# Kernel tuning notes

Measured on AMD Instinct MI355X. Metric: run time of the kernel, lower is better.

The kernel has to match this reference:

```python
import jax, jax.numpy as jnp
import numpy as np

H = 8
DA, DP, DK = 2048, 1024, 1024
B, N = 4, 2048
DOUT = 512
INNER = (DA + DP + DK) // H  # 512 = heads*dim_head


def setup_inputs() -> dict:
    key = jax.random.key(0)
    ks = jax.random.split(key, 7)
    x = jax.random.normal(ks[0], (B, N, DA + DP + DK), jnp.float32)
    mask = jax.random.randint(ks[1], (B, 1, N, N), 0, 2, jnp.int32)
    W_a = jax.random.normal(ks[2], (3 * DA // H, DA), jnp.float32) * (DA ** -0.5)
    W_p = jax.random.normal(ks[3], (3 * DP // H, DP), jnp.float32) * (DP ** -0.5)
    W_k = jax.random.normal(ks[4], (3 * DK // H, DK), jnp.float32) * (DK ** -0.5)
    W_out = jax.random.normal(ks[5], (DOUT, INNER), jnp.float32) * (INNER ** -0.5)
    b_out = jnp.zeros((DOUT,), jnp.float32)
    return {"x": x, "W_a": W_a, "W_p": W_p, "W_k": W_k,
            "W_out": W_out, "b_out": b_out, "mask": mask}


def _heads(t):  # [b, n, h*d] -> [b, h, n, d]
    b, n, hd = t.shape
    return t.reshape(b, n, H, hd // H).transpose(0, 2, 1, 3)


def reference(x, W_a, W_p, W_k, W_out, b_out, mask):
    # three branch QKV projections (each branch sees its own slice of x)
    qkv_a = x[..., :DA] @ W_a.T                      # [b, n, 3*DA/H]
    qkv_p = x[..., DA:DA + DP] @ W_p.T               # [b, n, 3*DP/H]
    qkv_k = x[..., DA + DP:] @ W_k.T                 # [b, n, 3*DK/H]
    q_a, k_a, v_a = [_heads(t) for t in jnp.split(qkv_a, 3, axis=-1)]
    q_p, k_p, v_p = [_heads(t) for t in jnp.split(qkv_p, 3, axis=-1)]
    q_k, k_k, v_k = [_heads(t) for t in jnp.split(qkv_k, 3, axis=-1)]

    m = mask > 0                                     # [b, 1, n, n]
    neg = jnp.asarray(-1e10, x.dtype)

    def branch(q, k, d):
        dots = jnp.einsum('bhid,bhjd->bhij', q, k) * (d ** -0.5)
        return jax.nn.softmax(jnp.where(m, dots, neg), axis=-1)

    # betas = [1,1,1] normalized -> 1/3 each (the nn.Parameters are unused in fwd)
    attn = (branch(q_a, k_a, DA) + branch(q_p, k_p, DP) + branch(q_k, k_k, DK)) / 3.0

    v = jnp.concatenate([v_a, v_p, v_k], axis=-1)    # [b, h, n, INNER/H]
    out = jnp.einsum('bhij,bhjd->bhid', attn, v)     # [b, h, n, INNER/H]
    out = out.transpose(0, 2, 1, 3).reshape(x.shape[0], x.shape[1], INNER)
    return out @ W_out.T + b_out
```

## Files before the change

kernel.cpp:

```cpp
#include <hip/hip_runtime.h>
#include <hip/hip_bf16.h>

typedef __attribute__((ext_vector_type(8))) __bf16 bf16x8;
typedef __attribute__((ext_vector_type(4))) float f32x4;
typedef unsigned short u16;
typedef unsigned int u32;
typedef unsigned long long u64;

__device__ __forceinline__ u32 cvtpk(float lo, float hi) {
  u32 r;
  asm("v_cvt_pk_bf16_f32 %0, %1, %2" : "=v"(r) : "v"(lo), "v"(hi));
  return r;
}
__device__ __forceinline__ float rexp2(float x) {
  float r;
  asm("v_exp_f32 %0, %1" : "=v"(r) : "v"(x));
  return r;
}
__device__ __forceinline__ void gl_lds16(const void* g, void* l) {
  __builtin_amdgcn_global_load_lds((const __attribute__((address_space(1))) void*)g,
                                   (__attribute__((address_space(3))) void*)l, 16, 0, 0);
}
__device__ __forceinline__ int sigma_inv(int n) {
  return ((n >> 5) << 5) | (((n & 15) >> 2) << 3) | ((n & 3) << 1) | ((n >> 4) & 1);
}

__global__ __launch_bounds__(256) void prep_kernel(
    const float* __restrict__ x, u16* __restrict__ xb,
    const float* __restrict__ Wa, const float* __restrict__ Wp,
    const float* __restrict__ Wk, const float* __restrict__ Wo,
    u16* __restrict__ Wab, u16* __restrict__ Wpb,
    u16* __restrict__ Wkb, u16* __restrict__ Wob,
    const int* __restrict__ mask, u64* __restrict__ bits, int xblocks) {
  int bid = blockIdx.x;
  if (bid < xblocks) {
    const int idx = (bid * 256 + threadIdx.x) * 16;
    const float4 a0 = *(const float4*)(x + idx);
    const float4 a1 = *(const float4*)(x + idx + 4);
    const float4 a2 = *(const float4*)(x + idx + 8);
    const float4 a3 = *(const float4*)(x + idx + 12);
    uint4 t0, t1;
    t0.x = cvtpk(a0.x, a0.y); t0.y = cvtpk(a0.z, a0.w);
    t0.z = cvtpk(a1.x, a1.y); t0.w = cvtpk(a1.z, a1.w);
    t1.x = cvtpk(a2.x, a2.y); t1.y = cvtpk(a2.z, a2.w);
    t1.z = cvtpk(a3.x, a3.y); t1.w = cvtpk(a3.z, a3.w);
    *(uint4*)(xb + idx) = t0;
    *(uint4*)(xb + idx + 8) = t1;
    return;
  }
  bid -= xblocks;
  if (bid < 2560) {
    const float* s; u16* d; int base;
    if (bid < 1536)      { s = Wa; d = Wab; base = bid; }
    else if (bid < 1920) { s = Wp; d = Wpb; base = bid - 1536; }
    else if (bid < 2304) { s = Wk; d = Wkb; base = bid - 1920; }
    else                 { s = Wo; d = Wob; base = bid - 2304; }
    const int idx = (base * 256 + threadIdx.x) * 4;
    const float4 v = *(const float4*)(s + idx);
    *(uint2*)(d + idx) = make_uint2(cvtpk(v.x, v.y), cvtpk(v.z, v.w));
    return;
  }
  bid -= 2560;
  const int lane = threadIdx.x & 63;
  const long long gw = (long long)bid * 4 + (threadIdx.x >> 6);
  const long long nwaves = 1024LL * 4;
  const long long nwords = 16777216LL / 64;
  for (long long i = gw; i < nwords; i += nwaves) {
    const int m = mask[i * 64 + lane];
    const u64 bal = __ballot(m > 0);
    if (lane == 0) bits[i] = bal;
  }
}

__device__ __forceinline__ void qk_store(
    float v0, float v1, float v2, float v3, int m_base, int c,
    int dhs, int seg, float fs,
    u16* __restrict__ Qb, u16* __restrict__ Kb) {
  const int which = c >> (3 + dhs);
  const float f = (which == 0) ? fs : 1.0f;
  const u32 r01 = cvtpk(v0 * f, v1 * f);
  const u32 r23 = cvtpk(v2 * f, v3 * f);
  const u16 bvv[4] = {(u16)r01, (u16)(r01 >> 16), (u16)r23, (u16)(r23 >> 16)};
  const int hd_mask = (8 << dhs) - 1;
  const int r = c & hd_mask;
  const int hh = r >> dhs;
  const int d = r & ((1 << dhs) - 1);
  #pragma unroll
  for (int j = 0; j < 4; ++j) {
    const int m = m_base + j;
    const int bb = m >> 11, n = m & 2047;
    const size_t bhn = (size_t)(bb * 8 + hh) * 2048 + n;
    const u16 bv = bvv[j];
    if (which == 0) Qb[bhn * 64 + seg + d] = bv;
    else            Kb[bhn * 64 + seg + d] = bv;
  }
}

__global__ __launch_bounds__(256) void qkv_gemm_kernel(
    const u16* __restrict__ xb, const u16* __restrict__ Wa,
    const u16* __restrict__ Wp, const u16* __restrict__ Wk,
    u16* __restrict__ Qb, u16* __restrict__ Kb, u16* __restrict__ Vt) {
  __shared__ u16 smem[64 * 64 + 128 * 64];
  u16* lA = smem;
  u16* lB = smem + 64 * 64;

  const int tid = threadIdx.x;
  const int w = tid >> 6, l = tid & 63;
  const int lr = l & 15, lg = l >> 4;

  const int wg = blockIdx.x;
  const int xcd = wg & 7;
  const int q = wg >> 3;
  const int mtl = q / 12, nt = q % 12;
  const int mt = (xcd << 4) + mtl;

  const u16* W; int xoff, Kd, col0, dhs, seg;
  if (nt < 6)      { W = Wa; xoff = 0;    Kd = 2048; col0 = nt * 128;       dhs = 5; seg = 0;  }
  else if (nt < 9) { W = Wp; xoff = 2048; Kd = 1024; col0 = (nt - 6) * 128; dhs = 4; seg = 32; }
  else             { W = Wk; xoff = 3072; Kd = 1024; col0 = (nt - 9) * 128; dhs = 4; seg = 48; }
  const float qscale = (dhs == 5) ? 0.031880107f : 0.045084220f;
  const bool isV = (nt == 4) | (nt == 5) | (nt == 8) | (nt == 11);

  const int m0 = mt * 64;
  f32x4 acc[4][2] = {};
  const int ubase = tid & ~63;

  const int nk = Kd >> 6;
  #pragma unroll 1
  for (int kt = 0; kt < nk; ++kt) {
    const int k0 = kt << 6;
    #pragma unroll
    for (int i = 0; i < 2; ++i) {
      const int ch = i * 256 + tid;
      const int row = ch >> 3, c8 = (ch & 7) << 3;
      gl_lds16(xb + (size_t)(m0 + row) * 4096 + xoff + k0 + c8,
               lA + (size_t)(i * 256 + ubase) * 8);
    }
    #pragma unroll
    for (int i = 0; i < 4; ++i) {
      const int ch = i * 256 + tid;
      const int row = ch >> 3, c8 = (ch & 7) << 3;
      gl_lds16(W + (size_t)(col0 + row) * Kd + k0 + c8,
               lB + (size_t)(i * 256 + ubase) * 8);
    }
    __syncthreads();
    bf16x8 af[4][2], bfr[2][2];
    #pragma unroll
    for (int mi = 0; mi < 4; ++mi) {
      af[mi][0] = *(const bf16x8*)(lA + (mi * 16 + lr) * 64 + lg * 8);
      af[mi][1] = *(const bf16x8*)(lA + (mi * 16 + lr) * 64 + 32 + lg * 8);
    }
    #pragma unroll
    for (int ni = 0; ni < 2; ++ni) {
      bfr[ni][0] = *(const bf16x8*)(lB + (w * 32 + ni * 16 + lr) * 64 + lg * 8);
      bfr[ni][1] = *(const bf16x8*)(lB + (w * 32 + ni * 16 + lr) * 64 + 32 + lg * 8);
    }
    #pragma unroll
    for (int mi = 0; mi < 4; ++mi)
      #pragma unroll
      for (int ni = 0; ni < 2; ++ni) {
        acc[mi][ni] = __builtin_amdgcn_mfma_f32_16x16x32_bf16(af[mi][0], bfr[ni][0], acc[mi][ni], 0, 0, 0);
        acc[mi][ni] = __builtin_amdgcn_mfma_f32_16x16x32_bf16(af[mi][1], bfr[ni][1], acc[mi][ni], 0, 0, 0);
      }
    __syncthreads();
  }

  if (!isV) {
    #pragma unroll
    for (int mi = 0; mi < 4; ++mi)
      #pragma unroll
      for (int ni = 0; ni < 2; ++ni)
        qk_store(acc[mi][ni][0], acc[mi][ni][1], acc[mi][ni][2], acc[mi][ni][3],
                 m0 + mi * 16 + lg * 4, col0 + w * 32 + ni * 16 + lr,
                 dhs, seg, qscale, Qb, Kb);
  } else {
    #pragma unroll
    for (int mi = 0; mi < 4; ++mi)
      #pragma unroll
      for (int ni = 0; ni < 2; ++ni) {
        const u32 r01 = cvtpk(acc[mi][ni][0], acc[mi][ni][1]);
        const u32 r23 = cvtpk(acc[mi][ni][2], acc[mi][ni][3]);
        const u16 bvv[4] = {(u16)r01, (u16)(r01 >> 16), (u16)r23, (u16)(r23 >> 16)};
        const int cl = w * 32 + ni * 16 + lr;
        #pragma unroll
        for (int j = 0; j < 4; ++j) {
          const int n = mi * 16 + lg * 4 + j;
          smem[cl * 72 + sigma_inv(n)] = bvv[j];
        }
      }
    __syncthreads();
    const int c = tid >> 1, half = (tid & 1) << 5;
    const int hd_mask = (8 << dhs) - 1;
    const int r = (col0 + c) & hd_mask;
    const int hh = r >> dhs, d = r & ((1 << dhs) - 1);
    const int bb = m0 >> 11, n0v = m0 & 2047;
    u16* dst = Vt + ((size_t)(bb * 8 + hh) * 64 + seg + d) * 2048 + n0v + half;
    const u16* srcl = smem + c * 72 + half;
    #pragma unroll
    for (int e = 0; e < 4; ++e)
      *(uint4*)(dst + e * 8) = *(const uint4*)(srcl + e * 8);
  }
}

__global__ __launch_bounds__(256) void qkv_gemm_f32_kernel(
    const float* __restrict__ x, const u16* __restrict__ Wa,
    const u16* __restrict__ Wp, const u16* __restrict__ Wk,
    u16* __restrict__ Qb, u16* __restrict__ Kb, u16* __restrict__ Vt) {
  __shared__ u16 lA[128 * 64];
  __shared__ u16 lB[128 * 64];

  const int tid = threadIdx.x;
  const int w = tid >> 6, l = tid & 63;
  const int lr = l & 15, lg = l >> 4;
  const int wr = w >> 1, wc = w & 1;

  const int wg = blockIdx.x;
  const int xcd = wg & 7;
  const int q = wg >> 3;
  const int mtl = q / 12, nt = q % 12;
  const int mt = (xcd << 3) + mtl;

  const u16* W; int xoff, Kd, col0, dhs, seg;
  if (nt < 6)      { W = Wa; xoff = 0;    Kd = 2048; col0 = nt * 128;       dhs = 5; seg = 0;  }
  else if (nt < 9) { W = Wp; xoff = 2048; Kd = 1024; col0 = (nt - 6) * 128; dhs = 4; seg = 32; }
  else             { W = Wk; xoff = 3072; Kd = 1024; col0 = (nt - 9) * 128; dhs = 4; seg = 48; }
  const float qscale = (dhs == 5) ? 0.031880107f : 0.045084220f;

  const int m0 = mt * 128;
  f32x4 acc[4][4] = {};
  const int ubase = tid & ~63;

  const int nk = Kd >> 6;
  #pragma unroll 1
  for (int kt = 0; kt < nk; ++kt) {
    const int k0 = kt << 6;
    #pragma unroll
    for (int i = 0; i < 4; ++i) {
      const int ch = i * 256 + tid;
      const int row = ch >> 3, c8 = (ch & 7) << 3;
      const float* src = x + (size_t)(m0 + row) * 4096 + xoff + k0 + c8;
      const float4 a0 = *(const float4*)(src);
      const float4 a1 = *(const float4*)(src + 4);
      uint4 t;
      t.x = cvtpk(a0.x, a0.y); t.y = cvtpk(a0.z, a0.w);
      t.z = cvtpk(a1.x, a1.y); t.w = cvtpk(a1.z, a1.w);
      *(uint4*)(lA + (size_t)row * 64 + c8) = t;
    }
    #pragma unroll
    for (int i = 0; i < 4; ++i) {
      const int ch = i * 256 + tid;
      const int row = ch >> 3, c8 = (ch & 7) << 3;
      gl_lds16(W + (size_t)(col0 + row) * Kd + k0 + c8,
               lB + (size_t)(i * 256 + ubase) * 8);
    }
    __syncthreads();
    bf16x8 af[4][2], bfr[4][2];
    #pragma unroll
    for (int mi = 0; mi < 4; ++mi) {
      af[mi][0] = *(const bf16x8*)(lA + (wr * 64 + mi * 16 + lr) * 64 + lg * 8);
      af[mi][1] = *(const bf16x8*)(lA + (wr * 64 + mi * 16 + lr) * 64 + 32 + lg * 8);
    }
    #pragma unroll
    for (int ni = 0; ni < 4; ++ni) {
      bfr[ni][0] = *(const bf16x8*)(lB + (wc * 64 + ni * 16 + lr) * 64 + lg * 8);
      bfr[ni][1] = *(const bf16x8*)(lB + (wc * 64 + ni * 16 + lr) * 64 + 32 + lg * 8);
    }
    #pragma unroll
    for (int mi = 0; mi < 4; ++mi)
      #pragma unroll
      for (int ni = 0; ni < 4; ++ni) {
        acc[mi][ni] = __builtin_amdgcn_mfma_f32_16x16x32_bf16(af[mi][0], bfr[ni][0], acc[mi][ni], 0, 0, 0);
        acc[mi][ni] = __builtin_amdgcn_mfma_f32_16x16x32_bf16(af[mi][1], bfr[ni][1], acc[mi][ni], 0, 0, 0);
      }
    __syncthreads();
  }
  #pragma unroll
  for (int mi = 0; mi < 4; ++mi)
    #pragma unroll
    for (int ni = 0; ni < 4; ++ni) {
      const int c = col0 + wc * 64 + ni * 16 + lr;
      const int which = c >> (3 + dhs);
      const float f = (which == 0) ? qscale : 1.0f;
      const u32 r01 = cvtpk(acc[mi][ni][0] * f, acc[mi][ni][1] * f);
      const u32 r23 = cvtpk(acc[mi][ni][2] * f, acc[mi][ni][3] * f);
      const u16 bvv[4] = {(u16)r01, (u16)(r01 >> 16), (u16)r23, (u16)(r23 >> 16)};
      const int hd_mask = (8 << dhs) - 1;
      const int r = c & hd_mask;
      const int hh = r >> dhs;
      const int d = r & ((1 << dhs) - 1);
      #pragma unroll
      for (int j = 0; j < 4; ++j) {
        const int m = m0 + wr * 64 + mi * 16 + lg * 4 + j;
        const int bb = m >> 11, n = m & 2047;
        const size_t bhn = (size_t)(bb * 8 + hh) * 2048 + n;
        const u16 bv = bvv[j];
        if (which == 0)      Qb[bhn * 64 + seg + d] = bv;
        else if (which == 1) Kb[bhn * 64 + seg + d] = bv;
        else Vt[((size_t)(bb * 8 + hh) * 64 + seg + d) * 2048 + (n & ~63) + sigma_inv(n & 63)] = bv;
      }
    }
}

__global__ __launch_bounds__(512) void attn_kernel(
    const u16* __restrict__ Qb, const u16* __restrict__ Kb,
    const u16* __restrict__ Vt, const u32* __restrict__ mbits,
    u16* __restrict__ aout) {
  struct SMem {
    u16 sK[2][64 * 64];
    u16 sV[2][64 * 64];
  };
  __shared__ SMem sm;

  const int tid = threadIdx.x;
  const int w = tid >> 6, l = tid & 63;
  const int lr = l & 15, lg = l >> 4;
  const int wg = blockIdx.x;
  const int xcd = wg & 7, rr0 = wg >> 3;
  const int bh = (xcd << 2) + (rr0 >> 4);
  const int qt = rr0 & 15;
  const int b = bh >> 3, h = bh & 7;
  const int q0 = qt << 7;
  const size_t bhN = (size_t)bh * 2048;
  const int ubase = tid & ~63;

  const u16* qrow = Qb + (bhN + q0 + w * 16 + lr) * 64;
  const bf16x8 qf_a  = *(const bf16x8*)(qrow + lg * 8);
  const bf16x8 qf_pk = *(const bf16x8*)(qrow + 32 + lg * 8);
  bf16x8 zero8 = {};
  const bf16x8 qf_p = (lg < 2) ? qf_pk : zero8;
  const bf16x8 qf_k = (lg < 2) ? zero8 : qf_pk;

  const u32* mptr = mbits + ((size_t)b * 2048 + q0 + w * 16 + lr) * 64;

  const int sr = tid >> 3, swd = tid & 7;
  const u16* kp = Kb + (bhN + sr) * 64 + (swd ^ (sr & 7)) * 8;
  const u16* vp = Vt + ((size_t)bh * 64 + sr) * 2048 + (swd ^ (sr & 7)) * 8;
  u16* dK[2] = { &sm.sK[0][0] + ubase * 8, &sm.sK[1][0] + ubase * 8 };
  u16* dV[2] = { &sm.sV[0][0] + ubase * 8, &sm.sV[1][0] + ubase * 8 };

  uint2 mkA = *(const uint2*)(mptr);
  uint2 mkB;
  gl_lds16(kp, dK[0]);
  gl_lds16(vp, dV[0]);

  bf16x8 vones;
  #pragma unroll
  for (int e = 0; e < 8; ++e) vones[e] = __builtin_bit_cast(__bf16, (u16)0x3F80);

  f32x4 oacc[3][4] = {};
  f32x4 osum[3] = {};
  const int c4 = (lg << 2);
  const int xk = lr & 7;

  auto body = [&](int kt, int cur, bool st, uint2 mkv, uint2* mknext) {
    if (st) {
      *mknext = *(const uint2*)(mptr + ((kt + 1) << 1));
      gl_lds16(kp + (size_t)(kt + 1) * 4096, dK[cur ^ 1]);
      gl_lds16(vp + (size_t)(kt + 1) * 64, dV[cur ^ 1]);
      asm volatile("s_waitcnt vmcnt(3)" ::: "memory");
    } else {
      asm volatile("s_waitcnt vmcnt(0)" ::: "memory");
    }
    __builtin_amdgcn_sched_barrier(0);
    __builtin_amdgcn_s_barrier();

    u32 msk[4][2];
    #pragma unroll
    for (int j = 0; j < 4; ++j) {
      const int c = c4 + j;
      const u32 u0 = (mkv.x >> c) & 0x00010001u;
      const u32 u1 = (mkv.y >> c) & 0x00010001u;
      msk[j][0] = (u0 << 16) - u0;
      msk[j][1] = (u1 << 16) - u1;
    }

    bf16x8 vb[4][2];
    #pragma unroll
    for (int ct = 0; ct < 4; ++ct) {
      const u16* vrow = &sm.sV[cur][0] + (ct * 16 + lr) * 64;
      vb[ct][0] = *(const bf16x8*)(vrow + (lg ^ xk) * 8);
      vb[ct][1] = *(const bf16x8*)(vrow + ((lg + 4) ^ xk) * 8);
    }

    const f32x4 fz = {0.f, 0.f, 0.f, 0.f};
    auto softpv = [&](f32x4 (&sacc)[4], int s) {
      uint4 pw0, pw1;
      u32* w0 = (u32*)&pw0; u32* w1 = (u32*)&pw1;
      #pragma unroll
      for (int j = 0; j < 4; ++j) {
        w0[j] = cvtpk(rexp2(sacc[0][j]), rexp2(sacc[1][j])) & msk[j][0];
        w1[j] = cvtpk(rexp2(sacc[2][j]), rexp2(sacc[3][j])) & msk[j][1];
      }
      const bf16x8 pa0 = __builtin_bit_cast(bf16x8, pw0);
      const bf16x8 pa1 = __builtin_bit_cast(bf16x8, pw1);
      __builtin_amdgcn_s_setprio(1);
      #pragma unroll
      for (int ct = 0; ct < 4; ++ct) {
        oacc[s][ct] = __builtin_amdgcn_mfma_f32_16x16x32_bf16(pa0, vb[ct][0], oacc[s][ct], 0, 0, 0);
        oacc[s][ct] = __builtin_amdgcn_mfma_f32_16x16x32_bf16(pa1, vb[ct][1], oacc[s][ct], 0, 0, 0);
      }
      osum[s] = __builtin_amdgcn_mfma_f32_16x16x32_bf16(pa0, vones, osum[s], 0, 0, 0);
      osum[s] = __builtin_amdgcn_mfma_f32_16x16x32_bf16(pa1, vones, osum[s], 0, 0, 0);
      __builtin_amdgcn_s_setprio(0);
    };

    {
      f32x4 sacc[4];
      __builtin_amdgcn_s_setprio(1);
      #pragma unroll
      for (int t = 0; t < 4; ++t) {
        const bf16x8 kf = *(const bf16x8*)(&sm.sK[cur][0] + (t * 16 + lr) * 64 + ((lg ^ xk) * 8));
        sacc[t] = __builtin_amdgcn_mfma_f32_16x16x32_bf16(kf, qf_a, fz, 0, 0, 0);
      }
      __builtin_amdgcn_s_setprio(0);
      softpv(sacc, 0);
    }
    {
      f32x4 sacc[4];
      __builtin_amdgcn_s_setprio(1);
      #pragma unroll
      for (int t = 0; t < 4; ++t) {
        const bf16x8 kf = *(const bf16x8*)(&sm.sK[cur][0] + (t * 16 + lr) * 64 + (((lg + 4) ^ xk) * 8));
        sacc[t] = __builtin_amdgcn_mfma_f32_16x16x32_bf16(kf, qf_p, fz, 0, 0, 0);
      }
      __builtin_amdgcn_s_setprio(0);
      softpv(sacc, 1);
    }
    {
      f32x4 sacc[4];
      __builtin_amdgcn_s_setprio(1);
      #pragma unroll
      for (int t = 0; t < 4; ++t) {
        const bf16x8 kf = *(const bf16x8*)(&sm.sK[cur][0] + (t * 16 + lr) * 64 + (((lg + 4) ^ xk) * 8));
        sacc[t] = __builtin_amdgcn_mfma_f32_16x16x32_bf16(kf, qf_k, fz, 0, 0, 0);
      }
      __builtin_amdgcn_s_setprio(0);
      softpv(sacc, 2);
    }

    __builtin_amdgcn_s_barrier();
  };

  #pragma unroll 1
  for (int it = 0; it < 16; ++it) {
    body(2 * it, 0, true, mkA, &mkB);
    body(2 * it + 1, 1, it < 15, mkB, &mkA);
  }

  float linv[3][4];
  #pragma unroll
  for (int s = 0; s < 3; ++s)
    #pragma unroll
    for (int j = 0; j < 4; ++j)
      linv[s][j] = 1.0f / (3.0f * osum[s][j] + 1e-30f);

  #pragma unroll
  for (int ct = 0; ct < 4; ++ct) {
    float vj[4];
    #pragma unroll
    for (int j = 0; j < 4; ++j)
      vj[j] = oacc[0][ct][j] * linv[0][j]
            + oacc[1][ct][j] * linv[1][j]
            + oacc[2][ct][j] * linv[2][j];
    const u32 r01 = cvtpk(vj[0], vj[1]);
    const u32 r23 = cvtpk(vj[2], vj[3]);
    const u16 bvv[4] = {(u16)r01, (u16)(r01 >> 16), (u16)r23, (u16)(r23 >> 16)};
    #pragma unroll
    for (int j = 0; j < 4; ++j) {
      const int row = q0 + w * 16 + lg * 4 + j;
      const int col = h * 64 + ct * 16 + lr;
      aout[((size_t)b * 2048 + row) * 512 + col] = bvv[j];
    }
  }
}

__global__ __launch_bounds__(256) void out_gemm_kernel(
    const u16* __restrict__ A, const u16* __restrict__ Wo,
    const float* __restrict__ bias, float* __restrict__ out) {
  __shared__ u16 lA[64 * 64];
  __shared__ u16 lB[64 * 64];

  const int tid = threadIdx.x;
  const int w = tid >> 6, l = tid & 63;
  const int lr = l & 15, lg = l >> 4;

  const int wg = blockIdx.x;
  const int xcd = wg & 7;
  const int q = wg >> 3;
  const int mt = (xcd << 4) + (q >> 3);
  const int nt = q & 7;
  const int col0 = nt * 64;
  const int m0 = mt * 64;
  f32x4 acc[4] = {};
  const int ubase = tid & ~63;

  #pragma unroll 1
  for (int kt = 0; kt < 8; ++kt) {
    const int k0 = kt << 6;
    #pragma unroll
    for (int i = 0; i < 2; ++i) {
      const int ch = i * 256 + tid;
      const int row = ch >> 3, c8 = (ch & 7) << 3;
      gl_lds16(A + (size_t)(m0 + row) * 512 + k0 + c8, lA + (size_t)(i * 256 + ubase) * 8);
    }
    #pragma unroll
    for (int i = 0; i < 2; ++i) {
      const int ch = i * 256 + tid;
      const int row = ch >> 3, c8 = (ch & 7) << 3;
      gl_lds16(Wo + (size_t)(col0 + row) * 512 + k0 + c8, lB + (size_t)(i * 256 + ubase) * 8);
    }
    __syncthreads();
    bf16x8 af[4][2], bfr[2];
    #pragma unroll
    for (int mi = 0; mi < 4; ++mi) {
      af[mi][0] = *(const bf16x8*)(lA + (mi * 16 + lr) * 64 + lg * 8);
      af[mi][1] = *(const bf16x8*)(lA + (mi * 16 + lr) * 64 + 32 + lg * 8);
    }
    bfr[0] = *(const bf16x8*)(lB + (w * 16 + lr) * 64 + lg * 8);
    bfr[1] = *(const bf16x8*)(lB + (w * 16 + lr) * 64 + 32 + lg * 8);
    #pragma unroll
    for (int mi = 0; mi < 4; ++mi) {
      acc[mi] = __builtin_amdgcn_mfma_f32_16x16x32_bf16(af[mi][0], bfr[0], acc[mi], 0, 0, 0);
      acc[mi] = __builtin_amdgcn_mfma_f32_16x16x32_bf16(af[mi][1], bfr[1], acc[mi], 0, 0, 0);
    }
    __syncthreads();
  }

  const int c = col0 + w * 16 + lr;
  const float bv = bias[c];
  #pragma unroll
  for (int mi = 0; mi < 4; ++mi)
    #pragma unroll
    for (int j = 0; j < 4; ++j) {
      const int m = m0 + mi * 16 + lg * 4 + j;
      out[(size_t)m * 512 + c] = acc[mi][j] + bv;
    }
}

extern "C" void kernel_launch(void* const* d_in, const int* in_sizes, int n_in,
                              void* d_out, int out_size, void* d_ws, size_t ws_size,
                              hipStream_t stream) {
  const float* x    = (const float*)d_in[0];
  const float* Wa   = (const float*)d_in[1];
  const float* Wp   = (const float*)d_in[2];
  const float* Wk   = (const float*)d_in[3];
  const float* Wo   = (const float*)d_in[4];
  const float* bo   = (const float*)d_in[5];
  const int* mask   = (const int*)d_in[6];
  float* out = (float*)d_out;

  char* ws = (char*)d_ws;
  u16* Wab = (u16*)ws;
  u16* Wpb = (u16*)(ws + 3145728);
  u16* Wkb = (u16*)(ws + 3932160);
  u16* Wob = (u16*)(ws + 4718592);
  u16* Qb  = (u16*)(ws + 5242880);
  u16* Kb  = (u16*)(ws + 13631488);
  u16* Vt  = (u16*)(ws + 22020096);
  u64* Mb  = (u64*)(ws + 30408704);
  u16* Ao  = (u16*)(ws + 32505856);
  u16* xb  = (u16*)(ws + 40894464);

  const bool use_xb = ws_size >= (size_t)40894464 + 67108864;
  const int xblocks = use_xb ? 8192 : 0;

  prep_kernel<<<xblocks + 2560 + 1024, 256, 0, stream>>>(
      x, xb, Wa, Wp, Wk, Wo, Wab, Wpb, Wkb, Wob, mask, (u64*)Mb, xblocks);
  if (use_xb) {
    qkv_gemm_kernel<<<1536, 256, 0, stream>>>(xb, Wab, Wpb, Wkb, Qb, Kb, Vt);
  } else {
    qkv_gemm_f32_kernel<<<768, 256, 0, stream>>>(x, Wab, Wpb, Wkb, Qb, Kb, Vt);
  }
  attn_kernel<<<512, 512, 0, stream>>>(Qb, Kb, Vt, (const u32*)Mb, Ao);
  out_gemm_kernel<<<1024, 256, 0, stream>>>(Ao, Wob, bo, out);
}
```

Baseline: 267.9 us.

## Deepen K/V LDS prefetch to a four-stage ring with distance two

```diff
diff --git a/kernel.cpp b/kernel.cpp
--- a/kernel.cpp
+++ b/kernel.cpp
@@ -306,8 +306,8 @@
     const u16* __restrict__ Vt, const u32* __restrict__ mbits,
     u16* __restrict__ aout) {
   struct SMem {
-    u16 sK[2][64 * 64];
-    u16 sV[2][64 * 64];
+    u16 sK[4][64 * 64];
+    u16 sV[4][64 * 64];
   };
   __shared__ SMem sm;
 
@@ -335,13 +335,16 @@
   const int sr = tid >> 3, swd = tid & 7;
   const u16* kp = Kb + (bhN + sr) * 64 + (swd ^ (sr & 7)) * 8;
   const u16* vp = Vt + ((size_t)bh * 64 + sr) * 2048 + (swd ^ (sr & 7)) * 8;
-  u16* dK[2] = { &sm.sK[0][0] + ubase * 8, &sm.sK[1][0] + ubase * 8 };
-  u16* dV[2] = { &sm.sV[0][0] + ubase * 8, &sm.sV[1][0] + ubase * 8 };
-
-  uint2 mkA = *(const uint2*)(mptr);
-  uint2 mkB;
-  gl_lds16(kp, dK[0]);
-  gl_lds16(vp, dV[0]);
+  u16* dK[4] = { &sm.sK[0][0] + ubase * 8, &sm.sK[1][0] + ubase * 8,
+                 &sm.sK[2][0] + ubase * 8, &sm.sK[3][0] + ubase * 8 };
+  u16* dV[4] = { &sm.sV[0][0] + ubase * 8, &sm.sV[1][0] + ubase * 8,
+                 &sm.sV[2][0] + ubase * 8, &sm.sV[3][0] + ubase * 8 };
+
+  gl_lds16(kp, dK[0]);               gl_lds16(vp, dV[0]);
+  gl_lds16(kp + 4096, dK[1]);        gl_lds16(vp + 64, dV[1]);
+  uint2 m0 = *(const uint2*)(mptr);
+  uint2 m1 = *(const uint2*)(mptr + 2);
+  uint2 m2, m3;
 
   bf16x8 vones;
   #pragma unroll
@@ -352,15 +355,15 @@
   const int c4 = (lg << 2);
   const int xk = lr & 7;
 
-  auto body = [&](int kt, int cur, bool st, uint2 mkv, uint2* mknext) {
-    if (st) {
-      *mknext = *(const uint2*)(mptr + ((kt + 1) << 1));
-      gl_lds16(kp + (size_t)(kt + 1) * 4096, dK[cur ^ 1]);
-      gl_lds16(vp + (size_t)(kt + 1) * 64, dV[cur ^ 1]);
-      asm volatile("s_waitcnt vmcnt(3)" ::: "memory");
-    } else {
-      asm volatile("s_waitcnt vmcnt(0)" ::: "memory");
-    }
+  auto body = [&](int kt, int cur, int sb, bool st2, int wc, uint2 mkv, uint2* mknext) {
+    if (st2) {
+      *mknext = *(const uint2*)(mptr + ((kt + 2) << 1));
+      gl_lds16(kp + (size_t)(kt + 2) * 4096, dK[sb]);
+      gl_lds16(vp + (size_t)(kt + 2) * 64, dV[sb]);
+    }
+    if (wc == 6)      asm volatile("s_waitcnt vmcnt(6)" ::: "memory");
+    else if (wc == 3) asm volatile("s_waitcnt vmcnt(3)" ::: "memory");
+    else              asm volatile("s_waitcnt vmcnt(0)" ::: "memory");
     __builtin_amdgcn_sched_barrier(0);
     __builtin_amdgcn_s_barrier();
 
@@ -437,14 +440,16 @@
       __builtin_amdgcn_s_setprio(0);
       softpv(sacc, 2);
     }
-
-    __builtin_amdgcn_s_barrier();
   };
 
   #pragma unroll 1
-  for (int it = 0; it < 16; ++it) {
-    body(2 * it, 0, true, mkA, &mkB);
-    body(2 * it + 1, 1, it < 15, mkB, &mkA);
+  for (int it = 0; it < 8; ++it) {
+    const int kt0 = it * 4;
+    const bool l7 = (it < 7);
+    body(kt0 + 0, 0, 2, true, (kt0 == 0) ? 3 : 6, m0, &m2);
+    body(kt0 + 1, 1, 3, true, 6, m1, &m3);
+    body(kt0 + 2, 2, 0, l7, l7 ? 6 : 3, m2, &m0);
+    body(kt0 + 3, 3, 1, l7, l7 ? 6 : 0, m3, &m1);
   }
 
   float linv[3][4];
```

New measurement: 262.2 us. -2.2%, faster.
